# Kernel tuning notes

Measured on AMD Instinct MI355X. Metric: run time of the kernel, lower is better.

The kernel has to match this reference:

```python
import jax
import jax.numpy as jnp
from jax import lax
import numpy as np

BATCH = 8192
FEATURE_DIM = 512
NUM_ATOMS = 4096
SPARSITY = 32


def setup_inputs() -> dict:
    key = jax.random.key(0)
    k1, k2 = jax.random.split(key)
    X = jax.random.normal(k1, (BATCH, FEATURE_DIM), dtype=jnp.float32)
    # xavier_uniform for [feature_dim, num_atoms]
    limit = float(np.sqrt(6.0 / (FEATURE_DIM + NUM_ATOMS)))
    dictionary = jax.random.uniform(
        k2, (FEATURE_DIM, NUM_ATOMS), dtype=jnp.float32, minval=-limit, maxval=limit
    )
    return {"X": X, "dictionary": dictionary, "sparsity": SPARSITY}


def _matching_pursuit_codes(x, D, sparsity):
    # x: [feature_dim], D: [feature_dim, num_atoms]
    num_atoms = D.shape[1]

    def step(carry, _):
        residual, codes = carry
        proj = residual @ D                      # [num_atoms]
        best = jnp.argmax(jnp.abs(proj))         # data-dependent atom pick
        coef = proj[best]
        codes = codes.at[best].add(coef)
        residual = residual - coef * lax.dynamic_index_in_dim(D, best, axis=1, keepdims=False)
        return (residual, codes), None

    init = (x, jnp.zeros((num_atoms,), dtype=x.dtype))
    (_, codes), _ = lax.scan(step, init, None, length=sparsity)
    return codes


def reference(X, dictionary, sparsity):
    # Greedy matching pursuit per sample, vectorized over the batch.
    codes = jax.vmap(lambda x: _matching_pursuit_codes(x, dictionary, sparsity))(X)
    # Original uses projections[best].item() -> codes are detached from autograd.
    codes = lax.stop_gradient(codes)
    recon = codes @ dictionary.T                 # [batch, feature_dim]
    return recon
```

## Files before the change

### kernel.cpp

```cpp
#include <hip/hip_runtime.h>


#define FD 512
#define NA 4096

typedef float f32x4 __attribute__((ext_vector_type(4)));

__device__ __forceinline__ f32x4 ntload4(const float* p) {
  return __builtin_nontemporal_load((const f32x4*)p);
}
__device__ __forceinline__ void ntstore4(float* p, f32x4 v) {
  __builtin_nontemporal_store(v, (f32x4*)p);
}

__global__ __launch_bounds__(1024) void k_transpose(const float* __restrict__ D,
                                                    float* __restrict__ DT) {
  __shared__ float tile[32][33];
  const int bx = blockIdx.x * 32;
  const int by = blockIdx.y * 32;
  const int tx = threadIdx.x, ty = threadIdx.y;
  tile[ty][tx] = D[(size_t)(by + ty) * NA + bx + tx];
  __syncthreads();
  DT[(size_t)(bx + ty) * FD + by + tx] = tile[tx][ty];
}

template <bool NT_STORE>
__global__ __launch_bounds__(256) void k_gemm_nn(const float* __restrict__ A,
                                                 const float* __restrict__ B,
                                                 float* __restrict__ C,
                                                 int M, int N, int K) {
#define TM 128
#define TN 128
#define TK 16
#define PADM 132
  __shared__ float As[TK][PADM];
  __shared__ float Bs[TK][TN];
  const int t = threadIdx.x;
  const int tx = t & 15, ty = t >> 4;
  const int bm = blockIdx.y * TM, bn = blockIdx.x * TN;
  float acc[8][8];
#pragma unroll
  for (int i = 0; i < 8; i++)
#pragma unroll
    for (int j = 0; j < 8; j++) acc[i][j] = 0.f;
  for (int kt = 0; kt < K; kt += TK) {
#pragma unroll
    for (int i = 0; i < 2; i++) {
      const int f = t + i * 256;
      const int row = f >> 2;
      const int kc = (f & 3) * 4;
      const float4 v = *(const float4*)(A + (size_t)(bm + row) * K + kt + kc);
      As[kc + 0][row] = v.x;
      As[kc + 1][row] = v.y;
      As[kc + 2][row] = v.z;
      As[kc + 3][row] = v.w;
    }
#pragma unroll
    for (int i = 0; i < 2; i++) {
      const int f = t + i * 256;
      const int kr = f >> 5;
      const int nc = (f & 31) * 4;
      *(float4*)(&Bs[kr][nc]) = *(const float4*)(B + (size_t)(kt + kr) * N + bn + nc);
    }
    __syncthreads();
#pragma unroll
    for (int k = 0; k < TK; k++) {
      float a[8], b[8];
      *(float4*)(a) = *(const float4*)(&As[k][ty * 4]);
      *(float4*)(a + 4) = *(const float4*)(&As[k][64 + ty * 4]);
      *(float4*)(b) = *(const float4*)(&Bs[k][tx * 4]);
      *(float4*)(b + 4) = *(const float4*)(&Bs[k][64 + tx * 4]);
#pragma unroll
      for (int i = 0; i < 8; i++)
#pragma unroll
        for (int j = 0; j < 8; j++) acc[i][j] = fmaf(a[i], b[j], acc[i][j]);
    }
    __syncthreads();
  }
#pragma unroll
  for (int ih = 0; ih < 2; ih++)
#pragma unroll
    for (int i = 0; i < 4; i++) {
      float* Crow = C + (size_t)(bm + ih * 64 + ty * 4 + i) * N + bn;
      if (NT_STORE) {
        ntstore4(Crow + tx * 4, *(const f32x4*)&acc[ih * 4 + i][0]);
        ntstore4(Crow + 64 + tx * 4, *(const f32x4*)&acc[ih * 4 + i][4]);
      } else {
        *(float4*)(Crow + tx * 4) = *(float4*)(&acc[ih * 4 + i][0]);
        *(float4*)(Crow + 64 + tx * 4) = *(float4*)(&acc[ih * 4 + i][4]);
      }
    }
}

template <bool HAVE_PROJ>
__global__ __launch_bounds__(64, 4) void k_mp64(const float* __restrict__ X,
                                                const float* __restrict__ D,
                                                const float* __restrict__ proj_g,
                                                const float* __restrict__ G,
                                                const float* __restrict__ DT,
                                                float* __restrict__ out,
                                                const int* __restrict__ spars_p) {
  const int s = blockIdx.x;
  const int l = threadIdx.x;
  int sp = spars_p[0];
  if (sp < 0) sp = 0;
  if (sp > 128) sp = 128;

  __shared__ int a_idx_sh[128];
  __shared__ float a_coef_sh[128];
  __shared__ float xsh[FD];

  float p[64];
  if (HAVE_PROJ) {
    const float* pr = proj_g + (size_t)s * NA;
#pragma unroll
    for (int q = 0; q < 16; q++) {
      const f32x4 v = ntload4(pr + (q * 64 + l) * 4);
      p[q * 4 + 0] = v[0];
      p[q * 4 + 1] = v[1];
      p[q * 4 + 2] = v[2];
      p[q * 4 + 3] = v[3];
    }
  } else {
    for (int i = l; i < FD; i += 64) xsh[i] = X[(size_t)s * FD + i];
    __syncthreads();
#pragma unroll
    for (int r = 0; r < 64; r++) p[r] = 0.f;
    for (int k = 0; k < FD; k++) {
      const float xv = xsh[k];
      const float4* Dr = (const float4*)(D + (size_t)k * NA);
#pragma unroll
      for (int q = 0; q < 16; q++) {
        const float4 dv = Dr[q * 64 + l];
        p[q * 4 + 0] = fmaf(xv, dv.x, p[q * 4 + 0]);
        p[q * 4 + 1] = fmaf(xv, dv.y, p[q * 4 + 1]);
        p[q * 4 + 2] = fmaf(xv, dv.z, p[q * 4 + 2]);
        p[q * 4 + 3] = fmaf(xv, dv.w, p[q * 4 + 3]);
      }
    }
  }

  float av[4];
  unsigned ap[4];
#pragma unroll
  for (int a = 0; a < 4; a++) {
    av[a] = -1.f;
    ap[a] = 0xffffffffu;
  }
#pragma unroll
  for (int q = 0; q < 16; q++) {
    const int a = q & 3;
#pragma unroll
    for (int j = 0; j < 4; j++) {
      const float f = p[q * 4 + j];
      const float af = fabsf(f);
      const unsigned pay =
          ((unsigned)(q * 256 + l * 4 + j) << 1) | (__float_as_uint(f) >> 31);
      if (af > av[a]) {
        av[a] = af;
        ap[a] = pay;
      }
    }
  }

  for (int it = 0; it < sp; it++) {
    float fa = av[0];
    unsigned pa = ap[0];
#pragma unroll
    for (int a = 1; a < 4; a++) {
      if (av[a] > fa || (av[a] == fa && ap[a] < pa)) {
        fa = av[a];
        pa = ap[a];
      }
    }
    unsigned long long key =
        ((unsigned long long)__float_as_uint(fa) << 32) | (unsigned)(~pa);
#pragma unroll
    for (int off = 1; off < 64; off <<= 1) {
      const unsigned long long ok = __shfl_xor(key, off);
      if (ok > key) key = ok;
    }
    const unsigned pay = ~(unsigned)key;
    const int best = pay >> 1;
    const float ba = __uint_as_float((unsigned)(key >> 32));
    const float coef = (pay & 1) ? -ba : ba;

    if (l == 0) {
      a_idx_sh[it] = best;
      a_coef_sh[it] = coef;
    }

#pragma unroll
    for (int a = 0; a < 4; a++) {
      av[a] = -1.f;
      ap[a] = 0xffffffffu;
    }
    const float4* Gr = (const float4*)(G + (size_t)best * NA);
#pragma unroll
    for (int h = 0; h < 2; h++) {
      float4 g[8];
#pragma unroll
      for (int q = 0; q < 8; q++) g[q] = Gr[(h * 8 + q) * 64 + l];
#pragma unroll
      for (int q = 0; q < 8; q++) {
        const int qq = h * 8 + q;
        const int a = qq & 3;
        float f0 = fmaf(-coef, g[q].x, p[qq * 4 + 0]);
        float f1 = fmaf(-coef, g[q].y, p[qq * 4 + 1]);
        float f2 = fmaf(-coef, g[q].z, p[qq * 4 + 2]);
        float f3 = fmaf(-coef, g[q].w, p[qq * 4 + 3]);
        p[qq * 4 + 0] = f0;
        p[qq * 4 + 1] = f1;
        p[qq * 4 + 2] = f2;
        p[qq * 4 + 3] = f3;
        const unsigned base = (unsigned)(qq * 256 + l * 4) << 1;
        const float a0 = fabsf(f0), a1 = fabsf(f1), a2 = fabsf(f2), a3 = fabsf(f3);
        if (a0 > av[a]) { av[a] = a0; ap[a] = base | 0 | (__float_as_uint(f0) >> 31); }
        if (a1 > av[a]) { av[a] = a1; ap[a] = base | 2 | (__float_as_uint(f1) >> 31); }
        if (a2 > av[a]) { av[a] = a2; ap[a] = base | 4 | (__float_as_uint(f2) >> 31); }
        if (a3 > av[a]) { av[a] = a3; ap[a] = base | 6 | (__float_as_uint(f3) >> 31); }
      }
    }
  }

  __syncthreads();
  float4 acc0 = make_float4(0.f, 0.f, 0.f, 0.f);
  float4 acc1 = make_float4(0.f, 0.f, 0.f, 0.f);
  for (int it = 0; it < sp; it++) {
    const float c = a_coef_sh[it];
    const float4* dr = (const float4*)(DT + (size_t)a_idx_sh[it] * FD);
    const float4 d0 = dr[l];
    const float4 d1 = dr[64 + l];
    acc0.x = fmaf(c, d0.x, acc0.x);
    acc0.y = fmaf(c, d0.y, acc0.y);
    acc0.z = fmaf(c, d0.z, acc0.z);
    acc0.w = fmaf(c, d0.w, acc0.w);
    acc1.x = fmaf(c, d1.x, acc1.x);
    acc1.y = fmaf(c, d1.y, acc1.y);
    acc1.z = fmaf(c, d1.z, acc1.z);
    acc1.w = fmaf(c, d1.w, acc1.w);
  }
  float* orow = out + (size_t)s * FD;
  ntstore4(orow + l * 4, (f32x4){acc0.x, acc0.y, acc0.z, acc0.w});
  ntstore4(orow + 256 + l * 4, (f32x4){acc1.x, acc1.y, acc1.z, acc1.w});
}

extern "C" void kernel_launch(void* const* d_in, const int* in_sizes, int n_in,
                              void* d_out, int out_size, void* d_ws, size_t ws_size,
                              hipStream_t stream) {
  const float* X = (const float*)d_in[0];
  const float* D = (const float*)d_in[1];
  const int* spars = (const int*)d_in[2];
  float* out = (float*)d_out;
  const int B = in_sizes[0] / FD;

  char* ws = (char*)d_ws;
  const size_t szDT = (size_t)NA * FD * 4;
  const size_t szG = (size_t)NA * NA * 4;
  const size_t szProj = (size_t)B * NA * 4;

  float* DT = (float*)ws;
  float* G = (float*)(ws + szDT);
  float* proj = (float*)(ws + szDT + szG);
  const size_t need_full = szDT + szG + szProj;

  k_transpose<<<dim3(NA / 32, FD / 32), dim3(32, 32), 0, stream>>>(D, DT);

  if (ws_size >= need_full) {
    k_gemm_nn<true><<<dim3(NA / TN, B / TM), 256, 0, stream>>>(X, D, proj, B, NA, FD);
    k_gemm_nn<false><<<dim3(NA / TN, NA / TM), 256, 0, stream>>>(DT, D, G, NA, NA, FD);
    k_mp64<true><<<B, 64, 0, stream>>>(X, D, proj, G, DT, out, spars);
  } else {
    k_gemm_nn<false><<<dim3(NA / TN, NA / TM), 256, 0, stream>>>(DT, D, G, NA, NA, FD);
    k_mp64<false><<<B, 64, 0, stream>>>(X, D, nullptr, G, DT, out, spars);
  }
}
```

Measured before the change: 1.181 ms.

## Compute only upper triangle of symmetric Gram matrix and mirror; use packed fp32 FMA

The Gram matrix D^T D is symmetric, so the GEMM now skips tiles below the diagonal and a new mirror kernel copies the upper tiles into the lower half by transposing through shared memory. This roughly halves the Gram GEMM's FLOPs at the cost of an extra read/write pass over about half of G. Separately, the GEMM inner loop is rewritten with two-wide float vectors and elementwise FMA so the compiler can emit packed fp32 FMA instructions. The packed FMA change also applies to the X*D projection GEMM.

```diff
diff --git a/kernel.cpp b/kernel.cpp
--- a/kernel.cpp
+++ b/kernel.cpp
@@ -4,7 +4,13 @@
 #define FD 512
 #define NA 4096
 
+#define TM 128
+#define TN 128
+#define TK 16
+#define PADM 132
+
 typedef float f32x4 __attribute__((ext_vector_type(4)));
+typedef float f32x2 __attribute__((ext_vector_type(2)));
 
 __device__ __forceinline__ f32x4 ntload4(const float* p) {
   return __builtin_nontemporal_load((const f32x4*)p);
@@ -24,25 +30,34 @@
   DT[(size_t)(bx + ty) * FD + by + tx] = tile[tx][ty];
 }
 
-template <bool NT_STORE>
+__global__ __launch_bounds__(1024) void k_mirror(float* __restrict__ G) {
+  const int bx = blockIdx.x, by = blockIdx.y;
+  if ((bx >> 2) <= (by >> 2)) return;
+  __shared__ float tile[32][33];
+  const int tx = threadIdx.x, ty = threadIdx.y;
+  tile[ty][tx] = G[(size_t)(by * 32 + ty) * NA + bx * 32 + tx];
+  __syncthreads();
+  G[(size_t)(bx * 32 + ty) * NA + by * 32 + tx] = tile[tx][ty];
+}
+
+template <bool NT_STORE, bool TRIANGLE>
 __global__ __launch_bounds__(256) void k_gemm_nn(const float* __restrict__ A,
                                                  const float* __restrict__ B,
                                                  float* __restrict__ C,
                                                  int M, int N, int K) {
-#define TM 128
-#define TN 128
-#define TK 16
-#define PADM 132
+  if (TRIANGLE && (int)blockIdx.x < (int)blockIdx.y) return;
   __shared__ float As[TK][PADM];
   __shared__ float Bs[TK][TN];
   const int t = threadIdx.x;
   const int tx = t & 15, ty = t >> 4;
   const int bm = blockIdx.y * TM, bn = blockIdx.x * TN;
-  float acc[8][8];
+
+  f32x2 acc2[8][4];
 #pragma unroll
   for (int i = 0; i < 8; i++)
 #pragma unroll
-    for (int j = 0; j < 8; j++) acc[i][j] = 0.f;
+    for (int j = 0; j < 4; j++) acc2[i][j] = (f32x2){0.f, 0.f};
+
   for (int kt = 0; kt < K; kt += TK) {
 #pragma unroll
     for (int i = 0; i < 2; i++) {
@@ -65,15 +80,25 @@
     __syncthreads();
 #pragma unroll
     for (int k = 0; k < TK; k++) {
-      float a[8], b[8];
+      float a[8];
+      f32x2 b2[4];
       *(float4*)(a) = *(const float4*)(&As[k][ty * 4]);
       *(float4*)(a + 4) = *(const float4*)(&As[k][64 + ty * 4]);
-      *(float4*)(b) = *(const float4*)(&Bs[k][tx * 4]);
-      *(float4*)(b + 4) = *(const float4*)(&Bs[k][64 + tx * 4]);
-#pragma unroll
-      for (int i = 0; i < 8; i++)
-#pragma unroll
-        for (int j = 0; j < 8; j++) acc[i][j] = fmaf(a[i], b[j], acc[i][j]);
+      {
+        const f32x2* bp0 = (const f32x2*)(&Bs[k][tx * 4]);
+        const f32x2* bp1 = (const f32x2*)(&Bs[k][64 + tx * 4]);
+        b2[0] = bp0[0];
+        b2[1] = bp0[1];
+        b2[2] = bp1[0];
+        b2[3] = bp1[1];
+      }
+#pragma unroll
+      for (int i = 0; i < 8; i++) {
+        const f32x2 ai = (f32x2){a[i], a[i]};
+#pragma unroll
+        for (int j = 0; j < 4; j++)
+          acc2[i][j] = __builtin_elementwise_fma(ai, b2[j], acc2[i][j]);
+      }
     }
     __syncthreads();
   }
@@ -82,12 +107,14 @@
 #pragma unroll
     for (int i = 0; i < 4; i++) {
       float* Crow = C + (size_t)(bm + ih * 64 + ty * 4 + i) * N + bn;
+      const f32x4 lo = *(const f32x4*)(&acc2[ih * 4 + i][0]);
+      const f32x4 hi = *(const f32x4*)(&acc2[ih * 4 + i][2]);
       if (NT_STORE) {
-        ntstore4(Crow + tx * 4, *(const f32x4*)&acc[ih * 4 + i][0]);
-        ntstore4(Crow + 64 + tx * 4, *(const f32x4*)&acc[ih * 4 + i][4]);
+        ntstore4(Crow + tx * 4, lo);
+        ntstore4(Crow + 64 + tx * 4, hi);
       } else {
-        *(float4*)(Crow + tx * 4) = *(float4*)(&acc[ih * 4 + i][0]);
-        *(float4*)(Crow + 64 + tx * 4) = *(float4*)(&acc[ih * 4 + i][4]);
+        *(f32x4*)(Crow + tx * 4) = lo;
+        *(f32x4*)(Crow + 64 + tx * 4) = hi;
       }
     }
 }
@@ -267,11 +294,13 @@
   k_transpose<<<dim3(NA / 32, FD / 32), dim3(32, 32), 0, stream>>>(D, DT);
 
   if (ws_size >= need_full) {
-    k_gemm_nn<true><<<dim3(NA / TN, B / TM), 256, 0, stream>>>(X, D, proj, B, NA, FD);
-    k_gemm_nn<false><<<dim3(NA / TN, NA / TM), 256, 0, stream>>>(DT, D, G, NA, NA, FD);
+    k_gemm_nn<true, false><<<dim3(NA / TN, B / TM), 256, 0, stream>>>(X, D, proj, B, NA, FD);
+    k_gemm_nn<false, true><<<dim3(NA / TN, NA / TM), 256, 0, stream>>>(DT, D, G, NA, NA, FD);
+    k_mirror<<<dim3(NA / 32, NA / 32), dim3(32, 32), 0, stream>>>(G);
     k_mp64<true><<<B, 64, 0, stream>>>(X, D, proj, G, DT, out, spars);
   } else {
-    k_gemm_nn<false><<<dim3(NA / TN, NA / TM), 256, 0, stream>>>(DT, D, G, NA, NA, FD);
+    k_gemm_nn<false, true><<<dim3(NA / TN, NA / TM), 256, 0, stream>>>(DT, D, G, NA, NA, FD);
+    k_mirror<<<dim3(NA / 32, NA / 32), dim3(32, 32), 0, stream>>>(G);
     k_mp64<false><<<B, 64, 0, stream>>>(X, D, nullptr, G, DT, out, spars);
   }
 }
```

Measured after the change: 1.173 ms (median of 2 runs). Within noise of the previous version (-0.7%).
